# Optimization experiments

Hardware: AMD Instinct MI355X
Metric: run time of the kernel (lower is better)

The kernel has to match this reference:

```python
import jax, jax.numpy as jnp
import numpy as np

NUM_HEADS = 8
FOCUSING_FACTOR = 3.0
EPS = 1e-6


def setup_inputs() -> dict:
    key = jax.random.key(0)
    ks = jax.random.split(key, 5)
    B, C, H, W = 16, 256, 64, 64
    hd = C // NUM_HEADS
    return {
        "x": jax.random.normal(ks[0], (B, C, H, W), jnp.float32),
        "qkv_w": jax.random.normal(ks[1], (3 * C, C), jnp.float32) * 0.02,
        "qkv_b": jnp.zeros((3 * C,), jnp.float32),
        "proj_w": jax.random.normal(ks[2], (C, C), jnp.float32) * 0.02,
        "proj_b": jnp.zeros((C,), jnp.float32),
        "dwc_w": jax.random.normal(ks[3], (hd, 1, 5, 5), jnp.float32) * 0.02,
        "dwc_b": jnp.zeros((hd,), jnp.float32),
        "scale": jnp.zeros((1, 1, C), jnp.float32),
    }


def reference(x, qkv_w, qkv_b, proj_w, proj_b, dwc_w, dwc_b, scale):
    B, C, H, W = x.shape
    N = H * W
    hd = C // NUM_HEADS

    # b c h w -> b (h w) c
    xf = x.reshape(B, C, N).transpose(0, 2, 1)
    qkv = xf @ qkv_w.T + qkv_b  # [B, N, 3C]
    q, k, v = jnp.split(qkv, 3, axis=-1)

    # focusing feature map
    q = jax.nn.relu(q) + EPS
    k = jax.nn.relu(k) + EPS
    sc = jax.nn.softplus(scale)
    q = q / sc
    k = k / sc
    q_norm = jnp.linalg.norm(q, axis=-1, keepdims=True)
    k_norm = jnp.linalg.norm(k, axis=-1, keepdims=True)
    # focusing_factor <= 6 branch
    q = q ** FOCUSING_FACTOR
    k = k ** FOCUSING_FACTOR
    q = q / jnp.linalg.norm(q, axis=-1, keepdims=True) * q_norm
    k = k / jnp.linalg.norm(k, axis=-1, keepdims=True) * k_norm

    # b n (h c) -> (b h) n c
    def to_heads(t):
        return t.reshape(B, N, NUM_HEADS, hd).transpose(0, 2, 1, 3).reshape(B * NUM_HEADS, N, hd)

    q, k, v = to_heads(q), to_heads(k), to_heads(v)

    i, j, c, d = N, N, hd, hd
    z = 1.0 / (jnp.einsum('bic,bc->bi', q, k.sum(axis=1)) + EPS)
    if i * j * (c + d) > c * d * (i + j):
        kv = jnp.einsum('bjc,bjd->bcd', k, v)  # [(BH), c, d]
        out = jnp.einsum('bic,bcd,bi->bid', q, kv, z)
    else:
        qk = jnp.einsum('bic,bjc->bij', q, k)
        out = jnp.einsum('bij,bjd,bi->bid', qk, v, z)

    # depthwise conv on v: b (w h) c -> b c w h (square map)
    num = int(N ** 0.5)
    fm = v.transpose(0, 2, 1).reshape(B * NUM_HEADS, hd, num, num)
    fm = jax.lax.conv_general_dilated(
        fm, dwc_w, window_strides=(1, 1), padding='SAME',
        feature_group_count=hd,
        dimension_numbers=('NCHW', 'OIHW', 'NCHW')) + dwc_b[None, :, None, None]
    fm = fm.reshape(B * NUM_HEADS, hd, N).transpose(0, 2, 1)
    out = out + fm

    # (b h) n c -> b n (h c)
    out = out.reshape(B, NUM_HEADS, N, hd).transpose(0, 2, 1, 3).reshape(B, N, C)
    out = out @ proj_w.T + proj_b
    # b (h w) c -> b c h w
    return out.transpose(0, 2, 1).reshape(B, C, H, W)
```

## Files before the change

kernel.cpp:

```cpp
#include <hip/hip_runtime.h>
#include <cmath>

#define B_   16
#define C_   256
#define HW_  64
#define N_   4096
#define NH_  8
#define HD_  32
#define M_   (B_ * N_)
#define QKVC (3 * C_)
#define EPS_ 1e-6f

typedef short bf16x8 __attribute__((ext_vector_type(8)));
typedef float f32x4 __attribute__((ext_vector_type(4)));
typedef unsigned int u32x4 __attribute__((ext_vector_type(4)));

__device__ __forceinline__ float b2f(unsigned short u) {
  union { unsigned int i; float f; } v;
  v.i = ((unsigned int)u) << 16;
  return v.f;
}
__device__ __forceinline__ float blo(unsigned int u) {
  union { unsigned int i; float f; } v; v.i = u << 16; return v.f;
}
__device__ __forceinline__ float bhi(unsigned int u) {
  union { unsigned int i; float f; } v; v.i = u & 0xffff0000u; return v.f;
}
__device__ __forceinline__ unsigned short f2b(float f) {
  union { float f; unsigned int i; } v;
  v.f = f;
  unsigned int r = v.i + 0x7FFFu + ((v.i >> 16) & 1u);
  return (unsigned short)(r >> 16);
}
__device__ __forceinline__ void gload_lds16(const void* g, void* l) {
  __builtin_amdgcn_global_load_lds(
      (const __attribute__((address_space(1))) void*)g,
      (__attribute__((address_space(3))) void*)l, 16, 0, 0);
}

__global__ __launch_bounds__(256) void k_cast_x(const float* __restrict__ x,
                                                unsigned short* __restrict__ xT) {
  __shared__ float t[32][33];
  const int n0 = blockIdx.x * 32, c0 = blockIdx.y * 32, b = blockIdx.z;
  const int tid = threadIdx.x;
  const int r = tid >> 3, g = (tid & 7) * 4;
  float4 v = *reinterpret_cast<const float4*>(
      &x[((size_t)(b * C_ + c0 + r)) * N_ + n0 + g]);
  t[r][g + 0] = v.x; t[r][g + 1] = v.y; t[r][g + 2] = v.z; t[r][g + 3] = v.w;
  __syncthreads();
  ushort4 o;
  o.x = f2b(t[g + 0][r]); o.y = f2b(t[g + 1][r]);
  o.z = f2b(t[g + 2][r]); o.w = f2b(t[g + 3][r]);
  *reinterpret_cast<ushort4*>(&xT[((size_t)(b * N_ + n0 + r)) * C_ + c0 + g]) = o;
}

__global__ __launch_bounds__(256) void k_cast_w(const float* __restrict__ w1,
                                                const float* __restrict__ w2,
                                                unsigned short* __restrict__ dst) {
  const int g4 = (blockIdx.x * 256 + threadIdx.x) * 4;
  float4 v;
  if (g4 < 196608) v = *reinterpret_cast<const float4*>(w1 + g4);
  else             v = *reinterpret_cast<const float4*>(w2 + (g4 - 196608));
  ushort4 o;
  o.x = f2b(v.x); o.y = f2b(v.y); o.z = f2b(v.z); o.w = f2b(v.w);
  *reinterpret_cast<ushort4*>(dst + g4) = o;
}

__global__ void k_prep_scale(const float* __restrict__ scale,
                             float* __restrict__ rsc) {
  const int c = threadIdx.x;
  rsc[c] = 1.f / log1pf(expf(scale[c]));
}

template <int LDA, int OUTMODE, int NCOL>
__global__ __launch_bounds__(256) void k_gemm(
    const unsigned short* __restrict__ A, const unsigned short* __restrict__ W,
    const float* __restrict__ bias, void* __restrict__ outp) {
  __shared__ unsigned short As[128 * 64];
  __shared__ unsigned short Bs[128 * 64];
  const int tid = threadIdx.x;
  const int wid = tid >> 6, lane = tid & 63;
  const int lin = blockIdx.x + blockIdx.y * 512;
  const int bandp = lin >> 3;
  const int rowb = bandp / NCOL;
  const int colb = bandp - rowb * NCOL;
  const int m0 = (((lin & 7) << 6) + rowb) * 128;
  const int col0 = colb * 128;
  const int wr = wid >> 1, wc = wid & 1;

  const int lrow = lane >> 3;
  const int sl = (lane & 7) ^ (lrow & 7);

  f32x4 acc[4][4];
#pragma unroll
  for (int i = 0; i < 4; ++i)
#pragma unroll
    for (int j = 0; j < 4; ++j) acc[i][j] = (f32x4){0.f, 0.f, 0.f, 0.f};

  for (int kt = 0; kt < 4; ++kt) {
    const int k0 = kt * 64;
#pragma unroll
    for (int q = 0; q < 4; ++q) {
      const int chunk = wid * 4 + q;
      const int row = chunk * 8 + lrow;
      gload_lds16(A + (size_t)(m0 + row) * LDA + k0 + sl * 8, &As[chunk * 512]);
      gload_lds16(W + (size_t)(col0 + row) * 256 + k0 + sl * 8, &Bs[chunk * 512]);
    }
    __syncthreads();

    bf16x8 fa[2][4], fb[2][4];
#pragma unroll
    for (int i = 0; i < 4; ++i) {
      const int ra = wr * 64 + i * 16 + (lane & 15);
      const int rb = wc * 64 + i * 16 + (lane & 15);
#pragma unroll
      for (int ks = 0; ks < 2; ++ks) {
        const int s = ks * 4 + (lane >> 4);
        fa[ks][i] = *reinterpret_cast<const bf16x8*>(
            &As[ra * 64 + ((s ^ (ra & 7)) * 8)]);
        fb[ks][i] = *reinterpret_cast<const bf16x8*>(
            &Bs[rb * 64 + ((s ^ (rb & 7)) * 8)]);
      }
    }
#pragma unroll
    for (int i = 0; i < 4; ++i)
#pragma unroll
      for (int j = 0; j < 4; ++j) {
        acc[i][j] = __builtin_amdgcn_mfma_f32_16x16x32_bf16(fa[0][i], fb[0][j],
                                                            acc[i][j], 0, 0, 0);
        acc[i][j] = __builtin_amdgcn_mfma_f32_16x16x32_bf16(fa[1][i], fb[1][j],
                                                            acc[i][j], 0, 0, 0);
      }
    __syncthreads();
  }

  if (OUTMODE == 0) {
    unsigned short* O = (unsigned short*)outp;
#pragma unroll
    for (int j = 0; j < 4; ++j) {
      const int colg = col0 + wc * 64 + j * 16 + (lane & 15);
      const float bb = bias[colg];
#pragma unroll
      for (int i = 0; i < 4; ++i) {
        const int mrow = m0 + wr * 64 + i * 16 + ((lane >> 4) << 2);
#pragma unroll
        for (int r = 0; r < 4; ++r)
          O[(size_t)(mrow + r) * QKVC + colg] = f2b(acc[i][j][r] + bb);
      }
    }
  } else {
    float* O = (float*)outp;
    const int b = m0 >> 12;
    const int nb0 = (m0 & 4095) + wr * 64;
#pragma unroll
    for (int j = 0; j < 4; ++j) {
      const int colg = col0 + wc * 64 + j * 16 + (lane & 15);
      const float bb = bias[colg];
#pragma unroll
      for (int i = 0; i < 4; ++i) {
        const int nb = nb0 + i * 16 + ((lane >> 4) << 2);
        f32x4 o = acc[i][j];
        o += bb;
        __builtin_nontemporal_store(
            o, reinterpret_cast<f32x4*>(&O[((size_t)(b * C_ + colg)) * N_ + nb]));
      }
    }
  }
}

__global__ __launch_bounds__(256) void k_focus(unsigned short* __restrict__ qkv,
                                               const float* __restrict__ rsc) {
  const int wave = threadIdx.x >> 6, lane = threadIdx.x & 63;
  const int t = blockIdx.x * 4 + wave;
  const size_t base = (size_t)t * QKVC + lane * 4;

  uint2 qu = *reinterpret_cast<const uint2*>(qkv + base);
  uint2 ku = *reinterpret_cast<const uint2*>(qkv + base + C_);
  const f32x4 rs = *reinterpret_cast<const f32x4*>(rsc + lane * 4);

  float q[4], k[4], q3[4], k3[4];
  q[0] = blo(qu.x); q[1] = bhi(qu.x); q[2] = blo(qu.y); q[3] = bhi(qu.y);
  k[0] = blo(ku.x); k[1] = bhi(ku.x); k[2] = blo(ku.y); k[3] = bhi(ku.y);

  float sq2 = 0.f, sq6 = 0.f, sk2 = 0.f, sk6 = 0.f;
#pragma unroll
  for (int i = 0; i < 4; ++i) {
    q[i] = (fmaxf(q[i], 0.f) + EPS_) * rs[i];
    k[i] = (fmaxf(k[i], 0.f) + EPS_) * rs[i];
    const float q2 = q[i] * q[i], k2 = k[i] * k[i];
    q3[i] = q2 * q[i];
    k3[i] = k2 * k[i];
    sq2 += q2; sk2 += k2;
    sq6 += q3[i] * q3[i];
    sk6 += k3[i] * k3[i];
  }
#pragma unroll
  for (int off = 1; off < 64; off <<= 1) {
    sq2 += __shfl_xor(sq2, off);
    sq6 += __shfl_xor(sq6, off);
    sk2 += __shfl_xor(sk2, off);
    sk6 += __shfl_xor(sk6, off);
  }
  const float fq = sqrtf(sq2 / sq6);
  const float fk = sqrtf(sk2 / sk6);

  uint2 oq, ok;
  oq.x = (unsigned int)f2b(q3[0] * fq) | ((unsigned int)f2b(q3[1] * fq) << 16);
  oq.y = (unsigned int)f2b(q3[2] * fq) | ((unsigned int)f2b(q3[3] * fq) << 16);
  ok.x = (unsigned int)f2b(k3[0] * fk) | ((unsigned int)f2b(k3[1] * fk) << 16);
  ok.y = (unsigned int)f2b(k3[2] * fk) | ((unsigned int)f2b(k3[3] * fk) << 16);
  *reinterpret_cast<uint2*>(qkv + base) = oq;
  *reinterpret_cast<uint2*>(qkv + base + C_) = ok;
}

__global__ __launch_bounds__(256) void k_kv_part(
    const unsigned short* __restrict__ qkv, float* __restrict__ kvp,
    float* __restrict__ ksp) {
  const int bh = blockIdx.x;
  const int chunk = blockIdx.y;
  const int b = bh >> 3, h = bh & 7;
  const int tid = threadIdx.x;
  __shared__ float ks[16][32];
  __shared__ float vs[16][32];
  const int c = tid >> 3;
  const int d0 = (tid & 7) * 4;
  float a0 = 0.f, a1 = 0.f, a2 = 0.f, a3 = 0.f;
  float ksum_acc = 0.f;

  const int sel = tid >> 7;
  const int f = (tid & 127) * 4;
  const int jj_l = f >> 5, cc_l = f & 31;

  const int j_end = chunk * 512 + 512;
  for (int j0 = chunk * 512; j0 < j_end; j0 += 16) {
    __syncthreads();
    {
      const size_t rb = ((size_t)(b * N_ + j0 + jj_l)) * QKVC +
                        (sel ? 2 * C_ : C_) + h * HD_ + cc_l;
      uint2 u = *reinterpret_cast<const uint2*>(qkv + rb);
      float* dst = sel ? &vs[jj_l][cc_l] : &ks[jj_l][cc_l];
      dst[0] = blo(u.x);
      dst[1] = bhi(u.x);
      dst[2] = blo(u.y);
      dst[3] = bhi(u.y);
    }
    __syncthreads();
#pragma unroll
    for (int jj = 0; jj < 16; ++jj) {
      const float kc = ks[jj][c];
      a0 += kc * vs[jj][d0 + 0];
      a1 += kc * vs[jj][d0 + 1];
      a2 += kc * vs[jj][d0 + 2];
      a3 += kc * vs[jj][d0 + 3];
    }
    if (tid < 32) {
#pragma unroll
      for (int jj = 0; jj < 16; ++jj) ksum_acc += ks[jj][tid];
    }
  }
  float* kvo = kvp + ((size_t)chunk * 128 + bh) * 1024 + c * 32 + d0;
  kvo[0] = a0; kvo[1] = a1; kvo[2] = a2; kvo[3] = a3;
  if (tid < 32) ksp[((size_t)chunk * 128 + bh) * 32 + tid] = ksum_acc;
}

__global__ __launch_bounds__(256) void k_attn_mfma(
    unsigned short* __restrict__ qkv, const float* __restrict__ kvp,
    const float* __restrict__ ksp) {
  const int bh = blockIdx.y;
  const int b = bh >> 3, h = bh & 7;
  const int tid = threadIdx.x;
  const int lane = tid & 63;
  const int r0 = blockIdx.x * 256 + (tid >> 6) * 64;

  __shared__ float kv_s[1024];
  __shared__ float ksum_s[32];
  for (int pp = tid; pp < 1024; pp += 256) {
    float s = 0.f;
#pragma unroll
    for (int ch = 0; ch < 8; ++ch)
      s += kvp[((size_t)ch * 128 + bh) * 1024 + pp];
    kv_s[pp] = s;
  }
  if (tid < 32) {
    float s = 0.f;
#pragma unroll
    for (int ch = 0; ch < 8; ++ch)
      s += ksp[((size_t)ch * 128 + bh) * 32 + tid];
    ksum_s[tid] = s;
  }
  __syncthreads();

  const int kb = (lane >> 4) * 8;
  const int col = lane & 15;
  bf16x8 bhi0, bhi1, blo0, blo1;
  float ks0[8];
#pragma unroll
  for (int t = 0; t < 8; ++t) {
    const float v0 = kv_s[(kb + t) * 32 + col];
    const float v1 = kv_s[(kb + t) * 32 + col + 16];
    const unsigned short h0 = f2b(v0), h1 = f2b(v1);
    ((unsigned short*)&bhi0)[t] = h0;
    ((unsigned short*)&bhi1)[t] = h1;
    ((unsigned short*)&blo0)[t] = f2b(v0 - b2f(h0));
    ((unsigned short*)&blo1)[t] = f2b(v1 - b2f(h1));
    ks0[t] = ksum_s[kb + t];
  }

#pragma unroll
  for (int rt = 0; rt < 4; ++rt) {
    const int row = r0 + rt * 16 + (lane & 15);
    const bf16x8 a = *reinterpret_cast<const bf16x8*>(
        qkv + (size_t)(b * N_ + row) * QKVC + h * HD_ + kb);
    float zp = 0.f;
#pragma unroll
    for (int t = 0; t < 8; ++t) zp += b2f(((const unsigned short*)&a)[t]) * ks0[t];
    zp += __shfl_xor(zp, 16);
    zp += __shfl_xor(zp, 32);
    const float z = 1.f / (zp + EPS_);

    f32x4 acc0 = {0.f, 0.f, 0.f, 0.f}, acc1 = {0.f, 0.f, 0.f, 0.f};
    acc0 = __builtin_amdgcn_mfma_f32_16x16x32_bf16(a, blo0, acc0, 0, 0, 0);
    acc1 = __builtin_amdgcn_mfma_f32_16x16x32_bf16(a, blo1, acc1, 0, 0, 0);
    acc0 = __builtin_amdgcn_mfma_f32_16x16x32_bf16(a, bhi0, acc0, 0, 0, 0);
    acc1 = __builtin_amdgcn_mfma_f32_16x16x32_bf16(a, bhi1, acc1, 0, 0, 0);

#pragma unroll
    for (int r = 0; r < 4; ++r) {
      const int rr = (lane >> 4) * 4 + r;
      const float zr = __shfl(z, rr);
      unsigned short* op =
          qkv + (size_t)(b * N_ + r0 + rt * 16 + rr) * QKVC + h * HD_;
      op[col] = f2b(acc0[r] * zr);
      op[col + 16] = f2b(acc1[r] * zr);
    }
  }
}

__global__ __launch_bounds__(256) void k_conv(
    unsigned short* __restrict__ qkv, const float* __restrict__ dwc_w,
    const float* __restrict__ dwc_b) {
  const int lin = blockIdx.x;
  const int g2 = (lin & 7) * 256 + (lin >> 3);
  const int bh = g2 >> 4;
  const int ig = g2 & 15;
  const int i0 = ig * 4;
  const int b = bh >> 3, h = bh & 7;
  const int tid = threadIdx.x;
  const int j = tid >> 2;
  const int g = tid & 3;
  const int d0 = g * 8;
  const int wave = tid >> 6, lane = tid & 63;

  __shared__ float w_s[800];
  __shared__ float b_s[32];
  __shared__ unsigned short v_s[8 * 64 * 32];

#pragma unroll
  for (int rr = 0; rr < 8; ++rr) {
    const int ii = i0 + rr - 2;
    if (ii < 0 || ii >= 64) continue;
    gload_lds16(qkv + ((size_t)(b * N_ + ii * 64 + wave * 16 + (lane >> 2))) * QKVC +
                    2 * C_ + h * HD_ + (lane & 3) * 8,
                &v_s[rr * 2048 + wave * 512]);
  }
  for (int p = tid; p < 800; p += 256)
    w_s[p] = dwc_w[(p & 31) * 25 + (p >> 5)];
  if (tid < 32) b_s[tid] = dwc_b[tid];
  __syncthreads();

#pragma unroll
  for (int r = 0; r < 4; ++r) {
    const int i = i0 + r;
    float fm[8];
#pragma unroll
    for (int dd = 0; dd < 8; ++dd) fm[dd] = b_s[d0 + dd];
#pragma unroll
    for (int kr = 0; kr < 5; ++kr) {
      const int ii = i + kr - 2;
      if (ii < 0 || ii >= 64) continue;
      const int lr = r + kr;
#pragma unroll
      for (int kj = 0; kj < 5; ++kj) {
        const int jj = j + kj - 2;
        if (jj < 0 || jj >= 64) continue;
        const unsigned int* vr = reinterpret_cast<const unsigned int*>(
            &v_s[lr * 2048 + jj * 32 + d0]);
        const float* wt = &w_s[(kr * 5 + kj) * 32 + d0];
#pragma unroll
        for (int p = 0; p < 4; ++p) {
          const unsigned int vu = vr[p];
          fm[2 * p + 0] += blo(vu) * wt[2 * p + 0];
          fm[2 * p + 1] += bhi(vu) * wt[2 * p + 1];
        }
      }
    }
    unsigned int* orow = reinterpret_cast<unsigned int*>(
        qkv + ((size_t)(b * N_ + i * 64 + j)) * QKVC + h * HD_ + d0);
    uint4 cur = *reinterpret_cast<const uint4*>(orow);
    unsigned int o[4] = {cur.x, cur.y, cur.z, cur.w};
#pragma unroll
    for (int p = 0; p < 4; ++p) {
      const unsigned int lo = f2b(blo(o[p]) + fm[2 * p + 0]);
      const unsigned int hi = f2b(bhi(o[p]) + fm[2 * p + 1]);
      o[p] = lo | (hi << 16);
    }
    *reinterpret_cast<uint4*>(orow) = make_uint4(o[0], o[1], o[2], o[3]);
  }
}

extern "C" void kernel_launch(void* const* d_in, const int* in_sizes, int n_in,
                              void* d_out, int out_size, void* d_ws,
                              size_t ws_size, hipStream_t stream) {
  (void)in_sizes; (void)n_in; (void)out_size; (void)ws_size;
  const float* x      = (const float*)d_in[0];
  const float* qkv_w  = (const float*)d_in[1];
  const float* qkv_b  = (const float*)d_in[2];
  const float* proj_w = (const float*)d_in[3];
  const float* proj_b = (const float*)d_in[4];
  const float* dwc_w  = (const float*)d_in[5];
  const float* dwc_b  = (const float*)d_in[6];
  const float* scale  = (const float*)d_in[7];
  float* out = (float*)d_out;

  char* w = (char*)d_ws;
  unsigned short* xT   = (unsigned short*)w; w += (size_t)M_ * C_ * 2;
  unsigned short* qkvb = (unsigned short*)w; w += (size_t)M_ * QKVC * 2;
  unsigned short* wq   = (unsigned short*)w; w += (size_t)(QKVC + C_) * C_ * 2;
  unsigned short* wp   = wq + (size_t)QKVC * C_;
  float* kvp   = (float*)w;                  w += (size_t)8 * 128 * 1024 * 4;
  float* ksp   = (float*)w;                  w += (size_t)8 * 128 * 32 * 4;
  float* rscb  = (float*)w;                  w += 256 * 4;

  k_prep_scale<<<1, 256, 0, stream>>>(scale, rscb);
  k_cast_x<<<dim3(N_ / 32, C_ / 32, B_), 256, 0, stream>>>(x, xT);
  k_cast_w<<<256, 256, 0, stream>>>(qkv_w, proj_w, wq);
  k_gemm<256, 0, 6><<<dim3(512, 6), 256, 0, stream>>>(
      xT, wq, qkv_b, (void*)qkvb);
  k_focus<<<M_ / 4, 256, 0, stream>>>(qkvb, rscb);
  k_kv_part<<<dim3(128, 8), 256, 0, stream>>>(qkvb, kvp, ksp);
  k_attn_mfma<<<dim3(N_ / 256, 128), 256, 0, stream>>>(qkvb, kvp, ksp);
  k_conv<<<2048, 256, 0, stream>>>(qkvb, dwc_w, dwc_b);
  k_gemm<768, 1, 2><<<dim3(512, 2), 256, 0, stream>>>(
      qkvb, wp, proj_b, (void*)out);
}
```

Measured before the change: 213.1 us.

## Double-buffer KV partial kernel with direct global-to-LDS bf16 loads

Rewrites the k_kv_part staging loop to load 64-row tiles of K and V as raw bf16 straight into LDS with gload_lds16, double-buffered so the next tile's load overlaps compute on the current one. Tiles are converted to float on read from shared memory, and the loop runs 8 iterations of 64 rows instead of 32 of 16, so there are fewer barriers. The k-sum is now accumulated by every thread and written by one thread per channel. This relies on gload_lds16 being defined in the unseen part of the file and on its per-lane LDS placement matching the row/segment layout. LDS reads of the bf16 V tile may also hit bank conflicts.

```diff
diff --git a/kernel.cpp b/kernel.cpp
--- a/kernel.cpp
+++ b/kernel.cpp
@@ -220,47 +220,51 @@
   const int chunk = blockIdx.y;
   const int b = bh >> 3, h = bh & 7;
   const int tid = threadIdx.x;
-  __shared__ float ks[16][32];
-  __shared__ float vs[16][32];
+  const int wave = tid >> 6;
+  __shared__ unsigned short ks[2][64 * 32];
+  __shared__ unsigned short vs[2][64 * 32];
+
   const int c = tid >> 3;
   const int d0 = (tid & 7) * 4;
-  float a0 = 0.f, a1 = 0.f, a2 = 0.f, a3 = 0.f;
-  float ksum_acc = 0.f;
-
-  const int sel = tid >> 7;
-  const int f = (tid & 127) * 4;
-  const int jj_l = f >> 5, cc_l = f & 31;
-
-  const int j_end = chunk * 512 + 512;
-  for (int j0 = chunk * 512; j0 < j_end; j0 += 16) {
+  const int row = tid >> 2;
+  const int seg = (tid & 3) * 8;
+  const int j0 = chunk * 512;
+
+  float a0 = 0.f, a1 = 0.f, a2 = 0.f, a3 = 0.f, ksum_acc = 0.f;
+
+#define KV_STAGE(buf, jt)                                                     \
+  {                                                                           \
+    const size_t rb =                                                         \
+        ((size_t)(b * N_ + (jt) + row)) * QKVC + h * HD_ + seg;               \
+    gload_lds16(qkv + rb + C_, &ks[buf][wave * 512]);                         \
+    gload_lds16(qkv + rb + 2 * C_, &vs[buf][wave * 512]);                     \
+  }
+
+  KV_STAGE(0, j0);
+  __syncthreads();
+
+  int cur = 0;
+  for (int t = 0; t < 8; ++t) {
+    if (t < 7) KV_STAGE(cur ^ 1, j0 + (t + 1) * 64);
+#pragma unroll 8
+    for (int jj = 0; jj < 64; ++jj) {
+      const float kc = b2f(ks[cur][jj * 32 + c]);
+      const uint2 vv =
+          *reinterpret_cast<const uint2*>(&vs[cur][jj * 32 + d0]);
+      a0 += kc * blo(vv.x);
+      a1 += kc * bhi(vv.x);
+      a2 += kc * blo(vv.y);
+      a3 += kc * bhi(vv.y);
+      ksum_acc += kc;
+    }
     __syncthreads();
-    {
-      const size_t rb = ((size_t)(b * N_ + j0 + jj_l)) * QKVC +
-                        (sel ? 2 * C_ : C_) + h * HD_ + cc_l;
-      uint2 u = *reinterpret_cast<const uint2*>(qkv + rb);
-      float* dst = sel ? &vs[jj_l][cc_l] : &ks[jj_l][cc_l];
-      dst[0] = blo(u.x);
-      dst[1] = bhi(u.x);
-      dst[2] = blo(u.y);
-      dst[3] = bhi(u.y);
-    }
-    __syncthreads();
-#pragma unroll
-    for (int jj = 0; jj < 16; ++jj) {
-      const float kc = ks[jj][c];
-      a0 += kc * vs[jj][d0 + 0];
-      a1 += kc * vs[jj][d0 + 1];
-      a2 += kc * vs[jj][d0 + 2];
-      a3 += kc * vs[jj][d0 + 3];
-    }
-    if (tid < 32) {
-#pragma unroll
-      for (int jj = 0; jj < 16; ++jj) ksum_acc += ks[jj][tid];
-    }
-  }
+    cur ^= 1;
+  }
+#undef KV_STAGE
+
   float* kvo = kvp + ((size_t)chunk * 128 + bh) * 1024 + c * 32 + d0;
   kvo[0] = a0; kvo[1] = a1; kvo[2] = a2; kvo[3] = a3;
-  if (tid < 32) ksp[((size_t)chunk * 128 + bh) * 32 + tid] = ksum_acc;
+  if ((tid & 7) == 0) ksp[((size_t)chunk * 128 + bh) * 32 + c] = ksum_acc;
 }
 
 __global__ __launch_bounds__(256) void k_attn_mfma(
```

Result: slower. 217.5 us (+2.1%).
